# Kernel optimization log

Hardware: AMD Instinct MI355X
Metric: run time of the kernel (lower is better)

## Reference

```python
import jax, jax.numpy as jnp
import numpy as np

N = 100000   # num nodes
E = 1200000  # num edges
D = 64       # embedding dim
K = 3        # propagation hops (alpha has K+1 entries)


def setup_inputs() -> dict:
    key = jax.random.key(0)
    k1, k2, k3 = jax.random.split(key, 3)
    edge_index = jax.random.randint(k1, (2, E), 0, N, dtype=jnp.int64)
    weight = jax.random.normal(k2, (N, D), dtype=jnp.float32)
    alpha = jax.random.uniform(k3, (K + 1,), dtype=jnp.float32)
    return {"edge_index": edge_index, "weight": weight, "alpha": alpha}


def reference(edge_index, weight, alpha):
    row = edge_index[0]  # source j
    col = edge_index[1]  # target i
    # symmetric normalization: in-degree over col, deg^-1/2 with inf -> 0
    deg = jax.ops.segment_sum(jnp.ones((E,), dtype=weight.dtype), col, num_segments=N)
    dinv = jnp.where(deg == 0, 0.0, deg ** -0.5)
    edge_w = dinv[row] * dinv[col]  # [E]

    out = weight * alpha[0]
    x = weight
    for k in range(1, K + 1):
        # gather-scale-scatter propagation hop
        msg = edge_w[:, None] * x[row]                      # [E, D]
        x = jax.ops.segment_sum(msg, col, num_segments=N)   # [N, D]
        out = out + x * alpha[k]

    # per-edge link scores: dot(out[src], out[dst])
    return jnp.sum(out[row] * out[col], axis=-1)  # [E]
```

## Files before the change

kernel.cpp:

```cpp
#include <hip/hip_runtime.h>
#include <hip/hip_bf16.h>

#define GN 100000
#define GE 1200000
#define GD 64
#define NG 256
#define CPG 391
#define CAP 6144
#define PADCAP 12032
#define ZROFF (GN << 7)


__global__ void detect_kernel(const void* __restrict__ w,
                              const void* __restrict__ edge,
                              int* __restrict__ flags, int* __restrict__ gcount,
                              __hip_bfloat16* __restrict__ X,
                              __hip_bfloat16* __restrict__ Y) {
    __shared__ int s_badw, s_edgenz;
    if (threadIdx.x == 0) { s_badw = 0; s_edgenz = 0; }
    gcount[threadIdx.x] = 0;
    if (threadIdx.x < 16) {
        uint2 z; z.x = 0u; z.y = 0u;
        *(uint2*)(X + (size_t)GN * GD + 4 * threadIdx.x) = z;
        *(uint2*)(Y + (size_t)GN * GD + 4 * threadIdx.x) = z;
    }
    __syncthreads();
    const unsigned short* wh = (const unsigned short*)w;
    const unsigned int*   ei = (const unsigned int*)edge;
    int badw = 0, edgenz = 0;
    for (int i = threadIdx.x; i < 4096; i += 256) {
        unsigned int bits = ((unsigned int)wh[i]) << 16;
        float v = __uint_as_float(bits);
        if (!(fabsf(v) <= 100.0f)) badw = 1;
        if ((i & 1) == 1 && ei[i] != 0u) edgenz = 1;
    }
    if (badw)   atomicOr(&s_badw, 1);
    if (edgenz) atomicOr(&s_edgenz, 1);
    __syncthreads();
    if (threadIdx.x == 0) {
        flags[0] = s_badw ? 0 : 1;
        flags[1] = s_edgenz ? 0 : 1;
    }
}

__device__ __forceinline__ int ld_row(const int* __restrict__ edge, int e, int e64) {
    return e64 ? edge[2 * (size_t)e] : edge[e];
}
__device__ __forceinline__ int ld_col(const int* __restrict__ edge, int e, int e64) {
    return e64 ? edge[2 * ((size_t)GE + (size_t)e)] : edge[(size_t)GE + (size_t)e];
}
__device__ __forceinline__ float ld_f(const void* __restrict__ p, size_t i, int bf16f) {
    if (bf16f) return __bfloat162float(((const __hip_bfloat16*)p)[i]);
    return ((const float*)p)[i];
}

__device__ __forceinline__ float bf_lo(unsigned u) { return __uint_as_float(u << 16); }
__device__ __forceinline__ float bf_hi(unsigned u) { return __uint_as_float(u & 0xFFFF0000u); }
__device__ __forceinline__ unsigned bf16bits(float f) {
    __hip_bfloat16 h = __float2bfloat16(f);
    unsigned short s;
    __builtin_memcpy(&s, &h, 2);
    return (unsigned)s;
}

__global__ void p1init_kernel(const int* __restrict__ edge, const int* __restrict__ flags,
                              int* __restrict__ gcount, unsigned* __restrict__ bucket,
                              int E, int chunk,
                              const void* __restrict__ w, const void* __restrict__ alpha,
                              __hip_bfloat16* __restrict__ OUT, int nd) {
    if (blockIdx.x < NG) {
        __shared__ int cnt[NG];
        __shared__ int base[NG];
        int t = threadIdx.x;
        int e64 = flags[1];
        cnt[t] = 0;
        __syncthreads();
        int lo = blockIdx.x * chunk;
        int hiE = min(lo + chunk, E);
        for (int e = lo + t; e < hiE; e += 256) {
            int c = ld_col(edge, e, e64);
            int r = ld_row(edge, e, e64);
            if ((unsigned)c < (unsigned)GN && (unsigned)r < (unsigned)GN)
                atomicAdd(&cnt[c / CPG], 1);
        }
        __syncthreads();
        int cv = cnt[t];
        base[t] = (cv > 0) ? atomicAdd(&gcount[t], cv) : 0;
        __syncthreads();
        cnt[t] = 0;
        __syncthreads();
        for (int e = lo + t; e < hiE; e += 256) {
            int c = ld_col(edge, e, e64);
            int r = ld_row(edge, e, e64);
            if ((unsigned)c < (unsigned)GN && (unsigned)r < (unsigned)GN) {
                int g = c / CPG;
                int idx = base[g] + atomicAdd(&cnt[g], 1);
                if (idx < CAP)
                    bucket[(size_t)g * CAP + idx] = ((unsigned)(c - g * CPG) << 17) | (unsigned)r;
            }
        }
    } else {
        int bid = blockIdx.x - NG;
        int i = 4 * (bid * 256 + (int)threadIdx.x);
        int wbf = flags[0];
        if (i < nd) {
            float a0 = ld_f(alpha, 0, wbf);
            float v0 = ld_f(w, i + 0, wbf);
            float v1 = ld_f(w, i + 1, wbf);
            float v2 = ld_f(w, i + 2, wbf);
            float v3 = ld_f(w, i + 3, wbf);
            uint2 oq;
            oq.x = (bf16bits(a0 * v1) << 16) | bf16bits(a0 * v0);
            oq.y = (bf16bits(a0 * v3) << 16) | bf16bits(a0 * v2);
            *(uint2*)(OUT + i) = oq;
        }
    }
}

__global__ void p2_kernel(const unsigned* __restrict__ bucket, const int* __restrict__ gcount,
                          int2* __restrict__ begend, float* __restrict__ dinv,
                          int* __restrict__ csr,
                          const void* __restrict__ w, const int* __restrict__ flags,
                          __hip_bfloat16* __restrict__ XS) {
    int g = blockIdx.x;
    int t = threadIdx.x;
    __shared__ int hist[512];
    __shared__ int s[512];
    __shared__ float sdv[512];
    hist[t] = 0; hist[t + 256] = 0;
    __syncthreads();
    int mg = gcount[g]; if (mg > CAP) mg = CAP;
    const unsigned* bk = bucket + (size_t)g * CAP;
    for (int idx = t; idx < mg; idx += 256)
        atomicAdd(&hist[bk[idx] >> 17], 1);
    __syncthreads();
    int h0 = hist[t], h1 = hist[t + 256];
    int p0 = (h0 + 15) & ~15;
    int p1 = (h1 + 15) & ~15;
    s[t] = p0; s[t + 256] = p1;
    __syncthreads();
    for (int off = 1; off < 512; off <<= 1) {
        int v0 = (t >= off) ? s[t - off] : 0;
        int v1 = (t + 256 >= off) ? s[t + 256 - off] : 0;
        __syncthreads();
        s[t] += v0; s[t + 256] += v1;
        __syncthreads();
    }
    int gb = g * PADCAP;
    int beg0 = gb + s[t] - p0;
    int beg1 = gb + s[t + 256] - p1;
    float dv0 = (h0 > 0) ? rsqrtf((float)h0) : 0.0f;
    float dv1 = (h1 > 0) ? rsqrtf((float)h1) : 0.0f;
    sdv[t] = dv0; sdv[t + 256] = dv1;
    int col0 = g * CPG + t;
    int col1 = col0 + 256;
    if (col0 < GN) {
        begend[col0] = make_int2(beg0, beg0 + p0);
        dinv[col0] = dv0;
    }
    if (t + 256 < CPG && col1 < GN) {
        begend[col1] = make_int2(beg1, beg1 + p1);
        dinv[col1] = dv1;
    }
    __syncthreads();
    hist[t] = s[t] - p0;
    hist[t + 256] = s[t + 256] - p1;
    __syncthreads();
    for (int idx = t; idx < mg; idx += 256) {
        unsigned u = bk[idx];
        int cl = u >> 17;
        int r  = (int)(u & 0x1FFFFu);
        int pos = gb + atomicAdd(&hist[cl], 1);
        csr[pos] = r << 7;
    }
    if (col0 < GN)
        for (int q = h0; q < p0; ++q) csr[beg0 + q] = ZROFF;
    if (t + 256 < CPG && col1 < GN)
        for (int q = h1; q < p1; ++q) csr[beg1 + q] = ZROFF;
    int lo = g * CPG;
    int ncols = min(CPG, GN - lo);
    int tot = ncols << 6;
    int wbf = flags[0];
    size_t gbase = (size_t)lo << 6;
    if (wbf) {
        const unsigned short* wp = (const unsigned short*)w;
        for (int idx = 4 * t; idx < tot; idx += 1024) {
            float dv = sdv[idx >> 6];
            size_t base = gbase + (size_t)idx;
            uint2 wv = *(const uint2*)(wp + base);
            uint2 o;
            o.x = (bf16bits(dv * bf_hi(wv.x)) << 16) | bf16bits(dv * bf_lo(wv.x));
            o.y = (bf16bits(dv * bf_hi(wv.y)) << 16) | bf16bits(dv * bf_lo(wv.y));
            *(uint2*)(XS + base) = o;
        }
    } else {
        const float* wp = (const float*)w;
        for (int idx = 4 * t; idx < tot; idx += 1024) {
            float dv = sdv[idx >> 6];
            size_t base = gbase + (size_t)idx;
            float4 wv = *(const float4*)(wp + base);
            uint2 o;
            o.x = (bf16bits(dv * wv.y) << 16) | bf16bits(dv * wv.x);
            o.y = (bf16bits(dv * wv.w) << 16) | bf16bits(dv * wv.z);
            *(uint2*)(XS + base) = o;
        }
    }
}

__device__ __forceinline__ void acc16(int rv, unsigned ioff, const char* __restrict__ xb,
                                      int h, float& f0, float& f1, float& f2, float& f3) {
    unsigned r0 = (unsigned)__shfl(rv, h,      16);
    unsigned r1 = (unsigned)__shfl(rv, 4 + h,  16);
    unsigned r2 = (unsigned)__shfl(rv, 8 + h,  16);
    unsigned r3 = (unsigned)__shfl(rv, 12 + h, 16);
    uint2 u0 = *(const uint2*)(xb + (r0 + ioff));
    uint2 u1 = *(const uint2*)(xb + (r1 + ioff));
    uint2 u2 = *(const uint2*)(xb + (r2 + ioff));
    uint2 u3 = *(const uint2*)(xb + (r3 + ioff));
    f0 += bf_lo(u0.x); f1 += bf_hi(u0.x); f2 += bf_lo(u0.y); f3 += bf_hi(u0.y);
    f0 += bf_lo(u1.x); f1 += bf_hi(u1.x); f2 += bf_lo(u1.y); f3 += bf_hi(u1.y);
    f0 += bf_lo(u2.x); f1 += bf_hi(u2.x); f2 += bf_lo(u2.y); f3 += bf_hi(u2.y);
    f0 += bf_lo(u3.x); f1 += bf_hi(u3.x); f2 += bf_lo(u3.y); f3 += bf_hi(u3.y);
}

__global__ void gather_kernel(const __hip_bfloat16* __restrict__ XS,
                              __hip_bfloat16* __restrict__ Y,
                              __hip_bfloat16* __restrict__ OUT,
                              const int2* __restrict__ begend, const int* __restrict__ csr,
                              const float* __restrict__ dinv,
                              const void* __restrict__ alpha, const int* __restrict__ flags,
                              int k, int store_y, int N, int W) {
    int t = blockIdx.x * blockDim.x + threadIdx.x;
    int wid = __builtin_amdgcn_readfirstlane(t >> 6);
    if (wid >= N) return;
    int lane = t & 63;
    int h = lane >> 4;
    int i = lane & 15;
    float a = ld_f(alpha, k, flags[0]);
    const char* xb = (const char*)XS;
    unsigned ioff = 8u * (unsigned)i;
    int node = wid;
    int2 be = begend[node];
    float dc = dinv[node];
    size_t obase = (size_t)node * GD + 4 * i;
    uint2 uo = *(const uint2*)(OUT + obase);
    int rv = csr[be.x + i];
    for (;;) {
        int nn = node + W;
        bool more = nn < N;
        int2 be_n = make_int2(0, 0);
        float dc_n = 0.0f;
        uint2 uo_n; uo_n.x = 0u; uo_n.y = 0u;
        int rv_n = 0;
        if (more) {
            be_n = begend[nn];
            dc_n = dinv[nn];
            uo_n = *(const uint2*)(OUT + (size_t)nn * GD + 4 * i);
        }
        float f0 = 0.0f, f1 = 0.0f, f2 = 0.0f, f3 = 0.0f;
        int j = be.x;
        if (j < be.y) {
            acc16(rv, ioff, xb, h, f0, f1, f2, f3);
            for (j += 16; j < be.y; j += 16)
                acc16(csr[j + i], ioff, xb, h, f0, f1, f2, f3);
        }
        if (more) rv_n = csr[be_n.x + i];
        f0 += __shfl_xor(f0, 16, 64); f0 += __shfl_xor(f0, 32, 64);
        f1 += __shfl_xor(f1, 16, 64); f1 += __shfl_xor(f1, 32, 64);
        f2 += __shfl_xor(f2, 16, 64); f2 += __shfl_xor(f2, 32, 64);
        f3 += __shfl_xor(f3, 16, 64); f3 += __shfl_xor(f3, 32, 64);
        f0 *= dc; f1 *= dc; f2 *= dc; f3 *= dc;
        if (h == 0) {
            if (store_y) {
                uint2 p;
                p.x = (bf16bits(dc * f1) << 16) | bf16bits(dc * f0);
                p.y = (bf16bits(dc * f3) << 16) | bf16bits(dc * f2);
                *(uint2*)(Y + obase) = p;
            }
            float o0 = fmaf(a, f0, bf_lo(uo.x));
            float o1 = fmaf(a, f1, bf_hi(uo.x));
            float o2 = fmaf(a, f2, bf_lo(uo.y));
            float o3 = fmaf(a, f3, bf_hi(uo.y));
            uint2 q;
            q.x = (bf16bits(o1) << 16) | bf16bits(o0);
            q.y = (bf16bits(o3) << 16) | bf16bits(o2);
            *(uint2*)(OUT + obase) = q;
        }
        if (!more) break;
        node = nn; be = be_n; dc = dc_n; uo = uo_n; rv = rv_n;
        obase = (size_t)node * GD + 4 * i;
    }
}

__device__ __forceinline__ float dot2_bf16(unsigned ua, unsigned ub) {
    return fmaf(bf_lo(ua), bf_lo(ub), bf_hi(ua) * bf_hi(ub));
}

__global__ void dot_kernel(const __hip_bfloat16* __restrict__ OUT,
                           const int* __restrict__ edge, const int* __restrict__ flags,
                           void* __restrict__ res, int E, int NQ) {
    int t = blockIdx.x * blockDim.x + threadIdx.x;
    int q = t >> 2;
    int sub = t & 3;
    if (q >= E) return;
    int e64 = flags[1];
    int wbf = flags[0];
    int e0 = q;
    int r0 = ld_row(edge, e0, e64);
    int c0 = ld_col(edge, e0, e64);
    float m0 = ((unsigned)r0 < (unsigned)GN && (unsigned)c0 < (unsigned)GN) ? 1.0f : 0.0f;
    unsigned rc = ((unsigned)r0 < (unsigned)GN) ? (unsigned)r0 : 0u;
    unsigned cc = ((unsigned)c0 < (unsigned)GN) ? (unsigned)c0 : 0u;
    const uint4* pa = (const uint4*)(OUT + (size_t)rc * GD + sub * 16);
    const uint4* pb = (const uint4*)(OUT + (size_t)cc * GD + sub * 16);
    uint4 a0 = pa[0], a1 = pa[1], b0 = pb[0], b1 = pb[1];
    int e1 = e0 + NQ;
    bool more1 = e1 < E;
    int r1 = 0, c1 = 0;
    if (more1) { r1 = ld_row(edge, e1, e64); c1 = ld_col(edge, e1, e64); }
    for (;;) {
        uint4 na0, na1, nb0, nb1;
        na0.x=na0.y=na0.z=na0.w=0u; na1=na0; nb0=na0; nb1=na0;
        float m1 = 0.0f;
        if (more1) {
            m1 = ((unsigned)r1 < (unsigned)GN && (unsigned)c1 < (unsigned)GN) ? 1.0f : 0.0f;
            unsigned rc1 = ((unsigned)r1 < (unsigned)GN) ? (unsigned)r1 : 0u;
            unsigned cc1 = ((unsigned)c1 < (unsigned)GN) ? (unsigned)c1 : 0u;
            const uint4* qa = (const uint4*)(OUT + (size_t)rc1 * GD + sub * 16);
            const uint4* qb = (const uint4*)(OUT + (size_t)cc1 * GD + sub * 16);
            na0 = qa[0]; na1 = qa[1]; nb0 = qb[0]; nb1 = qb[1];
        }
        int e2 = e1 + NQ;
        bool more2 = more1 && (e2 < E);
        int r2 = 0, c2 = 0;
        if (more2) { r2 = ld_row(edge, e2, e64); c2 = ld_col(edge, e2, e64); }
        float p = (((dot2_bf16(a0.x, b0.x) + dot2_bf16(a0.y, b0.y)) +
                    (dot2_bf16(a0.z, b0.z) + dot2_bf16(a0.w, b0.w))) +
                   ((dot2_bf16(a1.x, b1.x) + dot2_bf16(a1.y, b1.y)) +
                    (dot2_bf16(a1.z, b1.z) + dot2_bf16(a1.w, b1.w)))) * m0;
        p += __shfl_down(p, 2, 4);
        p += __shfl_down(p, 1, 4);
        if (sub == 0) {
            if (wbf) ((__hip_bfloat16*)res)[e0] = __float2bfloat16(p);
            else     ((float*)res)[e0] = p;
        }
        if (!more1) break;
        e0 = e1; m0 = m1;
        a0 = na0; a1 = na1; b0 = nb0; b1 = nb1;
        e1 = e2; more1 = more2; r1 = r2; c1 = c2;
    }
}

extern "C" void kernel_launch(void* const* d_in, const int* in_sizes, int n_in,
                              void* d_out, int out_size, void* d_ws, size_t ws_size,
                              hipStream_t stream) {
    const int E = GE, N = GN, ND = GN * GD;
    const int NDP = (GN + 1) * GD;

    const void* edge   = d_in[0];
    const void* weight = d_in[1];
    const void* alpha  = d_in[2];

    char* ws = (char*)d_ws;
    int*      flags     = (int*)ws;      ws += 256;
    int*      gcount    = (int*)ws;      ws += 1024;
    float*    dinv      = (float*)ws;    ws += (((size_t)N * 4 + 255) / 256) * 256;
    int2*     begend    = (int2*)ws;     ws += (((size_t)N * 8 + 255) / 256) * 256;
    unsigned* bucket    = (unsigned*)ws; ws += (size_t)NG * CAP * 4;
    int*      csr       = (int*)ws;      ws += (size_t)NG * PADCAP * 4;
    __hip_bfloat16* X   = (__hip_bfloat16*)ws; ws += (size_t)NDP * 2;
    __hip_bfloat16* Y   = (__hip_bfloat16*)ws; ws += (size_t)NDP * 2;
    __hip_bfloat16* OUT = (__hip_bfloat16*)ws; ws += (size_t)ND * 2;

    const int B = 256;

    detect_kernel<<<1, 256, 0, stream>>>(weight, edge, flags, gcount, X, Y);

    {
        const int chunk = (E + NG - 1) / NG;
        const int initBlocks = (ND / 4 + B - 1) / B;
        p1init_kernel<<<NG + initBlocks, B, 0, stream>>>(
            (const int*)edge, flags, gcount, bucket, E, chunk,
            weight, alpha, OUT, ND);
    }
    p2_kernel<<<NG, 256, 0, stream>>>(bucket, gcount, begend, dinv, csr,
                                      weight, flags, X);

    const int PB = 2048;
    const int W  = PB * (B / 64);
    gather_kernel<<<PB, B, 0, stream>>>(X, Y, OUT, begend, csr, dinv, alpha, flags, 1, 1, N, W);
    gather_kernel<<<PB, B, 0, stream>>>(Y, X, OUT, begend, csr, dinv, alpha, flags, 2, 1, N, W);
    gather_kernel<<<PB, B, 0, stream>>>(X, Y, OUT, begend, csr, dinv, alpha, flags, 3, 0, N, W);

    const int NQ = PB * B / 4;
    dot_kernel<<<PB, B, 0, stream>>>(OUT, (const int*)edge, flags, d_out, E, NQ);
}
```

Before: 245.3 us.

## Widen gather to 8 lanes per row with 16-byte loads and 8-padded CSR

The gather kernel now uses 8 lanes of 16-byte loads per neighbor row instead of 16 lanes of 8-byte loads, so each wavefront processes 8 neighbors at a time. Neighbor indices are fetched 64 at a time and broadcast with full-wave shuffles, and the final reduction uses three xor steps. CSR segments are padded to multiples of 8 instead of 16, which shrinks padding and the CSR footprint, and the init kernel writes 8 bf16 per thread. The goal is fewer memory instructions and less padded-edge work, at the cost of more accumulator registers, a longer reduction, and reads of index slots past the segment end, which the extra workspace slack covers.

Measured after the change: 276.2 us. 12.6% more time.

```diff
diff --git a/kernel.cpp b/kernel.cpp
--- a/kernel.cpp
+++ b/kernel.cpp
@@ -7,7 +7,7 @@
 #define NG 256
 #define CPG 391
 #define CAP 6144
-#define PADCAP 12032
+#define PADCAP 8960
 #define ZROFF (GN << 7)
 
 
@@ -101,7 +101,7 @@
         }
     } else {
         int bid = blockIdx.x - NG;
-        int i = 4 * (bid * 256 + (int)threadIdx.x);
+        int i = 8 * (bid * 256 + (int)threadIdx.x);
         int wbf = flags[0];
         if (i < nd) {
             float a0 = ld_f(alpha, 0, wbf);
@@ -109,10 +109,16 @@
             float v1 = ld_f(w, i + 1, wbf);
             float v2 = ld_f(w, i + 2, wbf);
             float v3 = ld_f(w, i + 3, wbf);
-            uint2 oq;
+            float v4 = ld_f(w, i + 4, wbf);
+            float v5 = ld_f(w, i + 5, wbf);
+            float v6 = ld_f(w, i + 6, wbf);
+            float v7 = ld_f(w, i + 7, wbf);
+            uint4 oq;
             oq.x = (bf16bits(a0 * v1) << 16) | bf16bits(a0 * v0);
             oq.y = (bf16bits(a0 * v3) << 16) | bf16bits(a0 * v2);
-            *(uint2*)(OUT + i) = oq;
+            oq.z = (bf16bits(a0 * v5) << 16) | bf16bits(a0 * v4);
+            oq.w = (bf16bits(a0 * v7) << 16) | bf16bits(a0 * v6);
+            *(uint4*)(OUT + i) = oq;
         }
     }
 }
@@ -135,8 +141,8 @@
         atomicAdd(&hist[bk[idx] >> 17], 1);
     __syncthreads();
     int h0 = hist[t], h1 = hist[t + 256];
-    int p0 = (h0 + 15) & ~15;
-    int p1 = (h1 + 15) & ~15;
+    int p0 = (h0 + 7) & ~7;
+    int p1 = (h1 + 7) & ~7;
     s[t] = p0; s[t + 256] = p1;
     __syncthreads();
     for (int off = 1; off < 512; off <<= 1) {
@@ -207,22 +213,6 @@
     }
 }
 
-__device__ __forceinline__ void acc16(int rv, unsigned ioff, const char* __restrict__ xb,
-                                      int h, float& f0, float& f1, float& f2, float& f3) {
-    unsigned r0 = (unsigned)__shfl(rv, h,      16);
-    unsigned r1 = (unsigned)__shfl(rv, 4 + h,  16);
-    unsigned r2 = (unsigned)__shfl(rv, 8 + h,  16);
-    unsigned r3 = (unsigned)__shfl(rv, 12 + h, 16);
-    uint2 u0 = *(const uint2*)(xb + (r0 + ioff));
-    uint2 u1 = *(const uint2*)(xb + (r1 + ioff));
-    uint2 u2 = *(const uint2*)(xb + (r2 + ioff));
-    uint2 u3 = *(const uint2*)(xb + (r3 + ioff));
-    f0 += bf_lo(u0.x); f1 += bf_hi(u0.x); f2 += bf_lo(u0.y); f3 += bf_hi(u0.y);
-    f0 += bf_lo(u1.x); f1 += bf_hi(u1.x); f2 += bf_lo(u1.y); f3 += bf_hi(u1.y);
-    f0 += bf_lo(u2.x); f1 += bf_hi(u2.x); f2 += bf_lo(u2.y); f3 += bf_hi(u2.y);
-    f0 += bf_lo(u3.x); f1 += bf_hi(u3.x); f2 += bf_lo(u3.y); f3 += bf_hi(u3.y);
-}
-
 __global__ void gather_kernel(const __hip_bfloat16* __restrict__ XS,
                               __hip_bfloat16* __restrict__ Y,
                               __hip_bfloat16* __restrict__ OUT,
@@ -234,61 +224,84 @@
     int wid = __builtin_amdgcn_readfirstlane(t >> 6);
     if (wid >= N) return;
     int lane = t & 63;
-    int h = lane >> 4;
-    int i = lane & 15;
+    int h = lane >> 3;
+    int i = lane & 7;
     float a = ld_f(alpha, k, flags[0]);
     const char* xb = (const char*)XS;
-    unsigned ioff = 8u * (unsigned)i;
+    unsigned ioff = 16u * (unsigned)i;
     int node = wid;
     int2 be = begend[node];
     float dc = dinv[node];
-    size_t obase = (size_t)node * GD + 4 * i;
-    uint2 uo = *(const uint2*)(OUT + obase);
-    int rv = csr[be.x + i];
+    size_t obase = (size_t)node * GD + 8 * i;
+    uint4 uo = *(const uint4*)(OUT + obase);
+    int rv = csr[be.x + lane];
     for (;;) {
         int nn = node + W;
         bool more = nn < N;
         int2 be_n = make_int2(0, 0);
         float dc_n = 0.0f;
-        uint2 uo_n; uo_n.x = 0u; uo_n.y = 0u;
+        uint4 uo_n; uo_n.x = uo_n.y = uo_n.z = uo_n.w = 0u;
         int rv_n = 0;
         if (more) {
             be_n = begend[nn];
             dc_n = dinv[nn];
-            uo_n = *(const uint2*)(OUT + (size_t)nn * GD + 4 * i);
-        }
-        float f0 = 0.0f, f1 = 0.0f, f2 = 0.0f, f3 = 0.0f;
-        int j = be.x;
-        if (j < be.y) {
-            acc16(rv, ioff, xb, h, f0, f1, f2, f3);
-            for (j += 16; j < be.y; j += 16)
-                acc16(csr[j + i], ioff, xb, h, f0, f1, f2, f3);
-        }
-        if (more) rv_n = csr[be_n.x + i];
-        f0 += __shfl_xor(f0, 16, 64); f0 += __shfl_xor(f0, 32, 64);
-        f1 += __shfl_xor(f1, 16, 64); f1 += __shfl_xor(f1, 32, 64);
-        f2 += __shfl_xor(f2, 16, 64); f2 += __shfl_xor(f2, 32, 64);
-        f3 += __shfl_xor(f3, 16, 64); f3 += __shfl_xor(f3, 32, 64);
+            uo_n = *(const uint4*)(OUT + (size_t)nn * GD + 8 * i);
+        }
+        float f0 = 0.f, f1 = 0.f, f2 = 0.f, f3 = 0.f;
+        float f4 = 0.f, f5 = 0.f, f6 = 0.f, f7 = 0.f;
+        int base = be.x;
+        for (;;) {
+            int cnt = min(64, be.y - base);
+            for (int s = 0; s < cnt; s += 8) {
+                unsigned r = (unsigned)__shfl(rv, s + h, 64);
+                uint4 u = *(const uint4*)(xb + (r + ioff));
+                f0 += bf_lo(u.x); f1 += bf_hi(u.x);
+                f2 += bf_lo(u.y); f3 += bf_hi(u.y);
+                f4 += bf_lo(u.z); f5 += bf_hi(u.z);
+                f6 += bf_lo(u.w); f7 += bf_hi(u.w);
+            }
+            base += 64;
+            if (base >= be.y) break;
+            rv = csr[base + lane];
+        }
+        if (more) rv_n = csr[be_n.x + lane];
+        f0 += __shfl_xor(f0, 8, 64); f0 += __shfl_xor(f0, 16, 64); f0 += __shfl_xor(f0, 32, 64);
+        f1 += __shfl_xor(f1, 8, 64); f1 += __shfl_xor(f1, 16, 64); f1 += __shfl_xor(f1, 32, 64);
+        f2 += __shfl_xor(f2, 8, 64); f2 += __shfl_xor(f2, 16, 64); f2 += __shfl_xor(f2, 32, 64);
+        f3 += __shfl_xor(f3, 8, 64); f3 += __shfl_xor(f3, 16, 64); f3 += __shfl_xor(f3, 32, 64);
+        f4 += __shfl_xor(f4, 8, 64); f4 += __shfl_xor(f4, 16, 64); f4 += __shfl_xor(f4, 32, 64);
+        f5 += __shfl_xor(f5, 8, 64); f5 += __shfl_xor(f5, 16, 64); f5 += __shfl_xor(f5, 32, 64);
+        f6 += __shfl_xor(f6, 8, 64); f6 += __shfl_xor(f6, 16, 64); f6 += __shfl_xor(f6, 32, 64);
+        f7 += __shfl_xor(f7, 8, 64); f7 += __shfl_xor(f7, 16, 64); f7 += __shfl_xor(f7, 32, 64);
         f0 *= dc; f1 *= dc; f2 *= dc; f3 *= dc;
+        f4 *= dc; f5 *= dc; f6 *= dc; f7 *= dc;
         if (h == 0) {
             if (store_y) {
-                uint2 p;
+                uint4 p;
                 p.x = (bf16bits(dc * f1) << 16) | bf16bits(dc * f0);
                 p.y = (bf16bits(dc * f3) << 16) | bf16bits(dc * f2);
-                *(uint2*)(Y + obase) = p;
+                p.z = (bf16bits(dc * f5) << 16) | bf16bits(dc * f4);
+                p.w = (bf16bits(dc * f7) << 16) | bf16bits(dc * f6);
+                *(uint4*)(Y + obase) = p;
             }
             float o0 = fmaf(a, f0, bf_lo(uo.x));
             float o1 = fmaf(a, f1, bf_hi(uo.x));
             float o2 = fmaf(a, f2, bf_lo(uo.y));
             float o3 = fmaf(a, f3, bf_hi(uo.y));
-            uint2 q;
+            float o4 = fmaf(a, f4, bf_lo(uo.z));
+            float o5 = fmaf(a, f5, bf_hi(uo.z));
+            float o6 = fmaf(a, f6, bf_lo(uo.w));
+            float o7 = fmaf(a, f7, bf_hi(uo.w));
+            uint4 q;
             q.x = (bf16bits(o1) << 16) | bf16bits(o0);
             q.y = (bf16bits(o3) << 16) | bf16bits(o2);
-            *(uint2*)(OUT + obase) = q;
+            q.z = (bf16bits(o5) << 16) | bf16bits(o4);
+            q.w = (bf16bits(o7) << 16) | bf16bits(o6);
+            *(uint4*)(OUT + obase) = q;
         }
         if (!more) break;
         node = nn; be = be_n; dc = dc_n; uo = uo_n; rv = rv_n;
-        obase = (size_t)node * GD + 4 * i;
+        obase = (size_t)node * GD + 8 * i;
     }
 }
 
@@ -367,7 +380,7 @@
     float*    dinv      = (float*)ws;    ws += (((size_t)N * 4 + 255) / 256) * 256;
     int2*     begend    = (int2*)ws;     ws += (((size_t)N * 8 + 255) / 256) * 256;
     unsigned* bucket    = (unsigned*)ws; ws += (size_t)NG * CAP * 4;
-    int*      csr       = (int*)ws;      ws += (size_t)NG * PADCAP * 4;
+    int*      csr       = (int*)ws;      ws += (size_t)NG * PADCAP * 4 + 256;
     __hip_bfloat16* X   = (__hip_bfloat16*)ws; ws += (size_t)NDP * 2;
     __hip_bfloat16* Y   = (__hip_bfloat16*)ws; ws += (size_t)NDP * 2;
     __hip_bfloat16* OUT = (__hip_bfloat16*)ws; ws += (size_t)ND * 2;
@@ -378,7 +391,7 @@
 
     {
         const int chunk = (E + NG - 1) / NG;
-        const int initBlocks = (ND / 4 + B - 1) / B;
+        const int initBlocks = (ND / 8 + B - 1) / B;
         p1init_kernel<<<NG + initBlocks, B, 0, stream>>>(
             (const int*)edge, flags, gcount, bucket, E, chunk,
             weight, alpha, OUT, ND);
```

## Assign contiguous node/edge ranges per wave and prefetch first neighbor rows

Applied to the files above, without the earlier changes.

Gather waves now process a contiguous block of nodes instead of a grid stride. They also issue the first 16 neighbor-row loads for the next node before finishing the current one, overlapping that latency with the reduction and store. The dot kernel likewise walks contiguous edge ranges per quad, and the init path writes 8 bf16 values per thread with 16-byte stores. Launch bounds are added to the gather kernel, and the csr buffer is padded so the speculative prefetch cannot read past its end. The prefetch adds register pressure, and contiguous partitioning can worsen load balance or coalescing of edge-index reads.

After: 272.6 us. +11.1%, slower.

```diff
diff --git a/kernel.cpp b/kernel.cpp
--- a/kernel.cpp
+++ b/kernel.cpp
@@ -101,7 +101,7 @@
         }
     } else {
         int bid = blockIdx.x - NG;
-        int i = 4 * (bid * 256 + (int)threadIdx.x);
+        int i = 8 * (bid * 256 + (int)threadIdx.x);
         int wbf = flags[0];
         if (i < nd) {
             float a0 = ld_f(alpha, 0, wbf);
@@ -109,10 +109,16 @@
             float v1 = ld_f(w, i + 1, wbf);
             float v2 = ld_f(w, i + 2, wbf);
             float v3 = ld_f(w, i + 3, wbf);
-            uint2 oq;
+            float v4 = ld_f(w, i + 4, wbf);
+            float v5 = ld_f(w, i + 5, wbf);
+            float v6 = ld_f(w, i + 6, wbf);
+            float v7 = ld_f(w, i + 7, wbf);
+            uint4 oq;
             oq.x = (bf16bits(a0 * v1) << 16) | bf16bits(a0 * v0);
             oq.y = (bf16bits(a0 * v3) << 16) | bf16bits(a0 * v2);
-            *(uint2*)(OUT + i) = oq;
+            oq.z = (bf16bits(a0 * v5) << 16) | bf16bits(a0 * v4);
+            oq.w = (bf16bits(a0 * v7) << 16) | bf16bits(a0 * v6);
+            *(uint4*)(OUT + i) = oq;
         }
     }
 }
@@ -223,35 +229,49 @@
     f0 += bf_lo(u3.x); f1 += bf_hi(u3.x); f2 += bf_lo(u3.y); f3 += bf_hi(u3.y);
 }
 
-__global__ void gather_kernel(const __hip_bfloat16* __restrict__ XS,
-                              __hip_bfloat16* __restrict__ Y,
-                              __hip_bfloat16* __restrict__ OUT,
-                              const int2* __restrict__ begend, const int* __restrict__ csr,
-                              const float* __restrict__ dinv,
-                              const void* __restrict__ alpha, const int* __restrict__ flags,
-                              int k, int store_y, int N, int W) {
+__global__ void __launch_bounds__(256, 8)
+gather_kernel(const __hip_bfloat16* __restrict__ XS,
+              __hip_bfloat16* __restrict__ Y,
+              __hip_bfloat16* __restrict__ OUT,
+              const int2* __restrict__ begend, const int* __restrict__ csr,
+              const float* __restrict__ dinv,
+              const void* __restrict__ alpha, const int* __restrict__ flags,
+              int k, int store_y, int N, int npw) {
     int t = blockIdx.x * blockDim.x + threadIdx.x;
     int wid = __builtin_amdgcn_readfirstlane(t >> 6);
-    if (wid >= N) return;
+    int n0 = wid * npw;
+    if (n0 >= N) return;
+    int nend = min(n0 + npw, N);
     int lane = t & 63;
     int h = lane >> 4;
     int i = lane & 15;
     float a = ld_f(alpha, k, flags[0]);
     const char* xb = (const char*)XS;
     unsigned ioff = 8u * (unsigned)i;
-    int node = wid;
+    int node = n0;
     int2 be = begend[node];
     float dc = dinv[node];
     size_t obase = (size_t)node * GD + 4 * i;
     uint2 uo = *(const uint2*)(OUT + obase);
     int rv = csr[be.x + i];
+    uint2 p0, p1, p2, p3;
+    p0.x = p0.y = p1.x = p1.y = p2.x = p2.y = p3.x = p3.y = 0u;
+    if (be.x < be.y) {
+        unsigned r0 = (unsigned)__shfl(rv, h,      16);
+        unsigned r1 = (unsigned)__shfl(rv, 4 + h,  16);
+        unsigned r2 = (unsigned)__shfl(rv, 8 + h,  16);
+        unsigned r3 = (unsigned)__shfl(rv, 12 + h, 16);
+        p0 = *(const uint2*)(xb + (r0 + ioff));
+        p1 = *(const uint2*)(xb + (r1 + ioff));
+        p2 = *(const uint2*)(xb + (r2 + ioff));
+        p3 = *(const uint2*)(xb + (r3 + ioff));
+    }
     for (;;) {
-        int nn = node + W;
-        bool more = nn < N;
+        int nn = node + 1;
+        bool more = nn < nend;
         int2 be_n = make_int2(0, 0);
         float dc_n = 0.0f;
         uint2 uo_n; uo_n.x = 0u; uo_n.y = 0u;
-        int rv_n = 0;
         if (more) {
             be_n = begend[nn];
             dc_n = dinv[nn];
@@ -260,16 +280,32 @@
         float f0 = 0.0f, f1 = 0.0f, f2 = 0.0f, f3 = 0.0f;
         int j = be.x;
         if (j < be.y) {
-            acc16(rv, ioff, xb, h, f0, f1, f2, f3);
+            f0 += bf_lo(p0.x); f1 += bf_hi(p0.x); f2 += bf_lo(p0.y); f3 += bf_hi(p0.y);
+            f0 += bf_lo(p1.x); f1 += bf_hi(p1.x); f2 += bf_lo(p1.y); f3 += bf_hi(p1.y);
+            f0 += bf_lo(p2.x); f1 += bf_hi(p2.x); f2 += bf_lo(p2.y); f3 += bf_hi(p2.y);
+            f0 += bf_lo(p3.x); f1 += bf_hi(p3.x); f2 += bf_lo(p3.y); f3 += bf_hi(p3.y);
             for (j += 16; j < be.y; j += 16)
                 acc16(csr[j + i], ioff, xb, h, f0, f1, f2, f3);
         }
+        int rv_n = 0;
         if (more) rv_n = csr[be_n.x + i];
         f0 += __shfl_xor(f0, 16, 64); f0 += __shfl_xor(f0, 32, 64);
         f1 += __shfl_xor(f1, 16, 64); f1 += __shfl_xor(f1, 32, 64);
         f2 += __shfl_xor(f2, 16, 64); f2 += __shfl_xor(f2, 32, 64);
         f3 += __shfl_xor(f3, 16, 64); f3 += __shfl_xor(f3, 32, 64);
         f0 *= dc; f1 *= dc; f2 *= dc; f3 *= dc;
+        uint2 q0, q1, q2, q3;
+        q0.x = q0.y = q1.x = q1.y = q2.x = q2.y = q3.x = q3.y = 0u;
+        if (more && be_n.x < be_n.y) {
+            unsigned r0 = (unsigned)__shfl(rv_n, h,      16);
+            unsigned r1 = (unsigned)__shfl(rv_n, 4 + h,  16);
+            unsigned r2 = (unsigned)__shfl(rv_n, 8 + h,  16);
+            unsigned r3 = (unsigned)__shfl(rv_n, 12 + h, 16);
+            q0 = *(const uint2*)(xb + (r0 + ioff));
+            q1 = *(const uint2*)(xb + (r1 + ioff));
+            q2 = *(const uint2*)(xb + (r2 + ioff));
+            q3 = *(const uint2*)(xb + (r3 + ioff));
+        }
         if (h == 0) {
             if (store_y) {
                 uint2 p;
@@ -287,7 +323,8 @@
             *(uint2*)(OUT + obase) = q;
         }
         if (!more) break;
-        node = nn; be = be_n; dc = dc_n; uo = uo_n; rv = rv_n;
+        node = nn; be = be_n; dc = dc_n; uo = uo_n;
+        p0 = q0; p1 = q1; p2 = q2; p3 = q3;
         obase = (size_t)node * GD + 4 * i;
     }
 }
@@ -298,14 +335,15 @@
 
 __global__ void dot_kernel(const __hip_bfloat16* __restrict__ OUT,
                            const int* __restrict__ edge, const int* __restrict__ flags,
-                           void* __restrict__ res, int E, int NQ) {
+                           void* __restrict__ res, int E, int epq) {
     int t = blockIdx.x * blockDim.x + threadIdx.x;
     int q = t >> 2;
     int sub = t & 3;
-    if (q >= E) return;
+    int e0 = q * epq;
+    if (e0 >= E) return;
+    int eend = min(e0 + epq, E);
     int e64 = flags[1];
     int wbf = flags[0];
-    int e0 = q;
     int r0 = ld_row(edge, e0, e64);
     int c0 = ld_col(edge, e0, e64);
     float m0 = ((unsigned)r0 < (unsigned)GN && (unsigned)c0 < (unsigned)GN) ? 1.0f : 0.0f;
@@ -314,8 +352,8 @@
     const uint4* pa = (const uint4*)(OUT + (size_t)rc * GD + sub * 16);
     const uint4* pb = (const uint4*)(OUT + (size_t)cc * GD + sub * 16);
     uint4 a0 = pa[0], a1 = pa[1], b0 = pb[0], b1 = pb[1];
-    int e1 = e0 + NQ;
-    bool more1 = e1 < E;
+    int e1 = e0 + 1;
+    bool more1 = e1 < eend;
     int r1 = 0, c1 = 0;
     if (more1) { r1 = ld_row(edge, e1, e64); c1 = ld_col(edge, e1, e64); }
     for (;;) {
@@ -330,8 +368,8 @@
             const uint4* qb = (const uint4*)(OUT + (size_t)cc1 * GD + sub * 16);
             na0 = qa[0]; na1 = qa[1]; nb0 = qb[0]; nb1 = qb[1];
         }
-        int e2 = e1 + NQ;
-        bool more2 = more1 && (e2 < E);
+        int e2 = e1 + 1;
+        bool more2 = more1 && (e2 < eend);
         int r2 = 0, c2 = 0;
         if (more2) { r2 = ld_row(edge, e2, e64); c2 = ld_col(edge, e2, e64); }
         float p = (((dot2_bf16(a0.x, b0.x) + dot2_bf16(a0.y, b0.y)) +
@@ -367,7 +405,7 @@
     float*    dinv      = (float*)ws;    ws += (((size_t)N * 4 + 255) / 256) * 256;
     int2*     begend    = (int2*)ws;     ws += (((size_t)N * 8 + 255) / 256) * 256;
     unsigned* bucket    = (unsigned*)ws; ws += (size_t)NG * CAP * 4;
-    int*      csr       = (int*)ws;      ws += (size_t)NG * PADCAP * 4;
+    int*      csr       = (int*)ws;      ws += (size_t)NG * PADCAP * 4 + 256;
     __hip_bfloat16* X   = (__hip_bfloat16*)ws; ws += (size_t)NDP * 2;
     __hip_bfloat16* Y   = (__hip_bfloat16*)ws; ws += (size_t)NDP * 2;
     __hip_bfloat16* OUT = (__hip_bfloat16*)ws; ws += (size_t)ND * 2;
@@ -378,7 +416,7 @@
 
     {
         const int chunk = (E + NG - 1) / NG;
-        const int initBlocks = (ND / 4 + B - 1) / B;
+        const int initBlocks = (ND / 8 + B - 1) / B;
         p1init_kernel<<<NG + initBlocks, B, 0, stream>>>(
             (const int*)edge, flags, gcount, bucket, E, chunk,
             weight, alpha, OUT, ND);
@@ -388,10 +426,12 @@
 
     const int PB = 2048;
     const int W  = PB * (B / 64);
-    gather_kernel<<<PB, B, 0, stream>>>(X, Y, OUT, begend, csr, dinv, alpha, flags, 1, 1, N, W);
-    gather_kernel<<<PB, B, 0, stream>>>(Y, X, OUT, begend, csr, dinv, alpha, flags, 2, 1, N, W);
-    gather_kernel<<<PB, B, 0, stream>>>(X, Y, OUT, begend, csr, dinv, alpha, flags, 3, 0, N, W);
+    const int npw = (N + W - 1) / W;
+    gather_kernel<<<PB, B, 0, stream>>>(X, Y, OUT, begend, csr, dinv, alpha, flags, 1, 1, N, npw);
+    gather_kernel<<<PB, B, 0, stream>>>(Y, X, OUT, begend, csr, dinv, alpha, flags, 2, 1, N, npw);
+    gather_kernel<<<PB, B, 0, stream>>>(X, Y, OUT, begend, csr, dinv, alpha, flags, 3, 0, N, npw);
 
     const int NQ = PB * B / 4;
-    dot_kernel<<<PB, B, 0, stream>>>(OUT, (const int*)edge, flags, d_out, E, NQ);
-}
+    const int epq = (E + NQ - 1) / NQ;
+    dot_kernel<<<PB, B, 0, stream>>>(OUT, (const int*)edge, flags, d_out, E, epq);
+}
```

## Fuse three propagation hops and dot into one cooperative persistent kernel

Applied to the files above, without the earlier changes.

Replaces the three gather launches and the dot launch with a single cooperative kernel that uses grid.sync between phases. Each wave keeps its partial OUT accumulator in registers across hops instead of re-reading and re-writing OUT in global memory, and writes OUT only in the final hop. The init path is also widened to 8 elements per thread with 16-byte stores. The costs are grid-wide barrier latency, register pressure from the per-node out[NPW] array (NPW=13 or 25), and a runtime occupancy check that falls back to the old path.

Result: slower. 252.0 us (+2.7%).

```diff
diff --git a/kernel.cpp b/kernel.cpp
--- a/kernel.cpp
+++ b/kernel.cpp
@@ -1,5 +1,6 @@
 #include <hip/hip_runtime.h>
 #include <hip/hip_bf16.h>
+#include <hip/hip_cooperative_groups.h>
 
 #define GN 100000
 #define GE 1200000
@@ -10,6 +11,8 @@
 #define PADCAP 12032
 #define ZROFF (GN << 7)
 
+
+namespace cg = cooperative_groups;
 
 __global__ void detect_kernel(const void* __restrict__ w,
                               const void* __restrict__ edge,
@@ -101,7 +104,7 @@
         }
     } else {
         int bid = blockIdx.x - NG;
-        int i = 4 * (bid * 256 + (int)threadIdx.x);
+        int i = 8 * (bid * 256 + (int)threadIdx.x);
         int wbf = flags[0];
         if (i < nd) {
             float a0 = ld_f(alpha, 0, wbf);
@@ -109,10 +112,16 @@
             float v1 = ld_f(w, i + 1, wbf);
             float v2 = ld_f(w, i + 2, wbf);
             float v3 = ld_f(w, i + 3, wbf);
-            uint2 oq;
+            float v4 = ld_f(w, i + 4, wbf);
+            float v5 = ld_f(w, i + 5, wbf);
+            float v6 = ld_f(w, i + 6, wbf);
+            float v7 = ld_f(w, i + 7, wbf);
+            uint4 oq;
             oq.x = (bf16bits(a0 * v1) << 16) | bf16bits(a0 * v0);
             oq.y = (bf16bits(a0 * v3) << 16) | bf16bits(a0 * v2);
-            *(uint2*)(OUT + i) = oq;
+            oq.z = (bf16bits(a0 * v5) << 16) | bf16bits(a0 * v4);
+            oq.w = (bf16bits(a0 * v7) << 16) | bf16bits(a0 * v6);
+            *(uint4*)(OUT + i) = oq;
         }
     }
 }
@@ -221,6 +230,160 @@
     f0 += bf_lo(u1.x); f1 += bf_hi(u1.x); f2 += bf_lo(u1.y); f3 += bf_hi(u1.y);
     f0 += bf_lo(u2.x); f1 += bf_hi(u2.x); f2 += bf_lo(u2.y); f3 += bf_hi(u2.y);
     f0 += bf_lo(u3.x); f1 += bf_hi(u3.x); f2 += bf_lo(u3.y); f3 += bf_hi(u3.y);
+}
+
+template<int NPW, bool FIRST, bool STORE, bool WOUT>
+__device__ __forceinline__ void hop_phase(const char* __restrict__ xb,
+        __hip_bfloat16* __restrict__ DST,
+        __hip_bfloat16* __restrict__ OUT,
+        const int2* __restrict__ begend, const int* __restrict__ csr,
+        const float* __restrict__ dinv, float a,
+        int wid, int W, int N, int h, int i, unsigned ioff,
+        uint2 (&out)[NPW])
+{
+    int node = wid;
+    int2 be = begend[node];
+    float dc = dinv[node];
+    size_t obase = (size_t)node * GD + 4 * i;
+    uint2 uo = FIRST ? *(const uint2*)(OUT + obase) : out[0];
+    int rv = csr[be.x + i];
+    #pragma unroll
+    for (int tt = 0; tt < NPW; ++tt) {
+        int nn = node + W;
+        bool more = (tt + 1 < NPW) && (nn < N);
+        int2 be_n = make_int2(0, 0);
+        float dc_n = 0.0f;
+        uint2 uo_n; uo_n.x = 0u; uo_n.y = 0u;
+        if (more) {
+            be_n = begend[nn];
+            dc_n = dinv[nn];
+            if (FIRST) uo_n = *(const uint2*)(OUT + (size_t)nn * GD + 4 * i);
+            else       uo_n = out[(tt + 1 < NPW) ? tt + 1 : 0];
+        }
+        float f0 = 0.0f, f1 = 0.0f, f2 = 0.0f, f3 = 0.0f;
+        int j = be.x;
+        if (j < be.y) {
+            acc16(rv, ioff, xb, h, f0, f1, f2, f3);
+            for (j += 16; j < be.y; j += 16)
+                acc16(csr[j + i], ioff, xb, h, f0, f1, f2, f3);
+        }
+        int rv_n = 0;
+        if (more) rv_n = csr[be_n.x + i];
+        f0 += __shfl_xor(f0, 16, 64); f0 += __shfl_xor(f0, 32, 64);
+        f1 += __shfl_xor(f1, 16, 64); f1 += __shfl_xor(f1, 32, 64);
+        f2 += __shfl_xor(f2, 16, 64); f2 += __shfl_xor(f2, 32, 64);
+        f3 += __shfl_xor(f3, 16, 64); f3 += __shfl_xor(f3, 32, 64);
+        f0 *= dc; f1 *= dc; f2 *= dc; f3 *= dc;
+        if (STORE && h == 0) {
+            uint2 p;
+            p.x = (bf16bits(dc * f1) << 16) | bf16bits(dc * f0);
+            p.y = (bf16bits(dc * f3) << 16) | bf16bits(dc * f2);
+            *(uint2*)(DST + obase) = p;
+        }
+        float o0 = fmaf(a, f0, bf_lo(uo.x));
+        float o1 = fmaf(a, f1, bf_hi(uo.x));
+        float o2 = fmaf(a, f2, bf_lo(uo.y));
+        float o3 = fmaf(a, f3, bf_hi(uo.y));
+        uint2 acc;
+        acc.x = (bf16bits(o1) << 16) | bf16bits(o0);
+        acc.y = (bf16bits(o3) << 16) | bf16bits(o2);
+        if (WOUT) {
+            if (h == 0) *(uint2*)(OUT + obase) = acc;
+        } else {
+            out[tt] = acc;
+        }
+        if (!more) break;
+        node = nn; be = be_n; dc = dc_n; uo = uo_n; rv = rv_n;
+        obase = (size_t)node * GD + 4 * i;
+    }
+}
+
+__device__ __forceinline__ float dot2_bf16(unsigned ua, unsigned ub) {
+    return fmaf(bf_lo(ua), bf_lo(ub), bf_hi(ua) * bf_hi(ub));
+}
+
+__device__ __forceinline__ void dot_body(const __hip_bfloat16* __restrict__ OUT,
+        const int* __restrict__ edge, int e64, int wbf,
+        void* __restrict__ res, int E, int NQ, int t) {
+    int q = t >> 2;
+    int sub = t & 3;
+    if (q >= E) return;
+    int e0 = q;
+    int r0 = ld_row(edge, e0, e64);
+    int c0 = ld_col(edge, e0, e64);
+    float m0 = ((unsigned)r0 < (unsigned)GN && (unsigned)c0 < (unsigned)GN) ? 1.0f : 0.0f;
+    unsigned rc = ((unsigned)r0 < (unsigned)GN) ? (unsigned)r0 : 0u;
+    unsigned cc = ((unsigned)c0 < (unsigned)GN) ? (unsigned)c0 : 0u;
+    const uint4* pa = (const uint4*)(OUT + (size_t)rc * GD + sub * 16);
+    const uint4* pb = (const uint4*)(OUT + (size_t)cc * GD + sub * 16);
+    uint4 a0 = pa[0], a1 = pa[1], b0 = pb[0], b1 = pb[1];
+    int e1 = e0 + NQ;
+    bool more1 = e1 < E;
+    int r1 = 0, c1 = 0;
+    if (more1) { r1 = ld_row(edge, e1, e64); c1 = ld_col(edge, e1, e64); }
+    for (;;) {
+        uint4 na0, na1, nb0, nb1;
+        na0.x=na0.y=na0.z=na0.w=0u; na1=na0; nb0=na0; nb1=na0;
+        float m1 = 0.0f;
+        if (more1) {
+            m1 = ((unsigned)r1 < (unsigned)GN && (unsigned)c1 < (unsigned)GN) ? 1.0f : 0.0f;
+            unsigned rc1 = ((unsigned)r1 < (unsigned)GN) ? (unsigned)r1 : 0u;
+            unsigned cc1 = ((unsigned)c1 < (unsigned)GN) ? (unsigned)c1 : 0u;
+            const uint4* qa = (const uint4*)(OUT + (size_t)rc1 * GD + sub * 16);
+            const uint4* qb = (const uint4*)(OUT + (size_t)cc1 * GD + sub * 16);
+            na0 = qa[0]; na1 = qa[1]; nb0 = qb[0]; nb1 = qb[1];
+        }
+        int e2 = e1 + NQ;
+        bool more2 = more1 && (e2 < E);
+        int r2 = 0, c2 = 0;
+        if (more2) { r2 = ld_row(edge, e2, e64); c2 = ld_col(edge, e2, e64); }
+        float p = (((dot2_bf16(a0.x, b0.x) + dot2_bf16(a0.y, b0.y)) +
+                    (dot2_bf16(a0.z, b0.z) + dot2_bf16(a0.w, b0.w))) +
+                   ((dot2_bf16(a1.x, b1.x) + dot2_bf16(a1.y, b1.y)) +
+                    (dot2_bf16(a1.z, b1.z) + dot2_bf16(a1.w, b1.w)))) * m0;
+        p += __shfl_down(p, 2, 4);
+        p += __shfl_down(p, 1, 4);
+        if (sub == 0) {
+            if (wbf) ((__hip_bfloat16*)res)[e0] = __float2bfloat16(p);
+            else     ((float*)res)[e0] = p;
+        }
+        if (!more1) break;
+        e0 = e1; m0 = m1;
+        a0 = na0; a1 = na1; b0 = nb0; b1 = nb1;
+        e1 = e2; more1 = more2; r1 = r2; c1 = c2;
+    }
+}
+
+template<int NPW, int WPE>
+__global__ void __launch_bounds__(256, WPE)
+fused_kernel(__hip_bfloat16* X, __hip_bfloat16* Y, __hip_bfloat16* OUT,
+             const int2* begend, const int* csr, const float* dinv,
+             const void* alpha, const int* flags,
+             const int* edge, void* res, int N, int E, int W)
+{
+    cg::grid_group grid = cg::this_grid();
+    int t = blockIdx.x * blockDim.x + threadIdx.x;
+    int wid = __builtin_amdgcn_readfirstlane(t >> 6);
+    int lane = t & 63;
+    int h = lane >> 4;
+    int i = lane & 15;
+    unsigned ioff = 8u * (unsigned)i;
+    int wbf = flags[0];
+    int e64 = flags[1];
+    float a1 = ld_f(alpha, 1, wbf);
+    float a2 = ld_f(alpha, 2, wbf);
+    float a3 = ld_f(alpha, 3, wbf);
+    uint2 out[NPW];
+    hop_phase<NPW, true,  true,  false>((const char*)X, Y, OUT, begend, csr, dinv, a1, wid, W, N, h, i, ioff, out);
+    __threadfence();
+    grid.sync();
+    hop_phase<NPW, false, true,  false>((const char*)Y, X, OUT, begend, csr, dinv, a2, wid, W, N, h, i, ioff, out);
+    __threadfence();
+    grid.sync();
+    hop_phase<NPW, false, false, true >((const char*)X, Y, OUT, begend, csr, dinv, a3, wid, W, N, h, i, ioff, out);
+    __threadfence();
+    grid.sync();
+    dot_body(OUT, edge, e64, wbf, res, E, (int)(gridDim.x * blockDim.x) / 4, t);
 }
 
 __global__ void gather_kernel(const __hip_bfloat16* __restrict__ XS,
@@ -292,63 +455,11 @@
     }
 }
 
-__device__ __forceinline__ float dot2_bf16(unsigned ua, unsigned ub) {
-    return fmaf(bf_lo(ua), bf_lo(ub), bf_hi(ua) * bf_hi(ub));
-}
-
 __global__ void dot_kernel(const __hip_bfloat16* __restrict__ OUT,
                            const int* __restrict__ edge, const int* __restrict__ flags,
                            void* __restrict__ res, int E, int NQ) {
     int t = blockIdx.x * blockDim.x + threadIdx.x;
-    int q = t >> 2;
-    int sub = t & 3;
-    if (q >= E) return;
-    int e64 = flags[1];
-    int wbf = flags[0];
-    int e0 = q;
-    int r0 = ld_row(edge, e0, e64);
-    int c0 = ld_col(edge, e0, e64);
-    float m0 = ((unsigned)r0 < (unsigned)GN && (unsigned)c0 < (unsigned)GN) ? 1.0f : 0.0f;
-    unsigned rc = ((unsigned)r0 < (unsigned)GN) ? (unsigned)r0 : 0u;
-    unsigned cc = ((unsigned)c0 < (unsigned)GN) ? (unsigned)c0 : 0u;
-    const uint4* pa = (const uint4*)(OUT + (size_t)rc * GD + sub * 16);
-    const uint4* pb = (const uint4*)(OUT + (size_t)cc * GD + sub * 16);
-    uint4 a0 = pa[0], a1 = pa[1], b0 = pb[0], b1 = pb[1];
-    int e1 = e0 + NQ;
-    bool more1 = e1 < E;
-    int r1 = 0, c1 = 0;
-    if (more1) { r1 = ld_row(edge, e1, e64); c1 = ld_col(edge, e1, e64); }
-    for (;;) {
-        uint4 na0, na1, nb0, nb1;
-        na0.x=na0.y=na0.z=na0.w=0u; na1=na0; nb0=na0; nb1=na0;
-        float m1 = 0.0f;
-        if (more1) {
-            m1 = ((unsigned)r1 < (unsigned)GN && (unsigned)c1 < (unsigned)GN) ? 1.0f : 0.0f;
-            unsigned rc1 = ((unsigned)r1 < (unsigned)GN) ? (unsigned)r1 : 0u;
-            unsigned cc1 = ((unsigned)c1 < (unsigned)GN) ? (unsigned)c1 : 0u;
-            const uint4* qa = (const uint4*)(OUT + (size_t)rc1 * GD + sub * 16);
-            const uint4* qb = (const uint4*)(OUT + (size_t)cc1 * GD + sub * 16);
-            na0 = qa[0]; na1 = qa[1]; nb0 = qb[0]; nb1 = qb[1];
-        }
-        int e2 = e1 + NQ;
-        bool more2 = more1 && (e2 < E);
-        int r2 = 0, c2 = 0;
-        if (more2) { r2 = ld_row(edge, e2, e64); c2 = ld_col(edge, e2, e64); }
-        float p = (((dot2_bf16(a0.x, b0.x) + dot2_bf16(a0.y, b0.y)) +
-                    (dot2_bf16(a0.z, b0.z) + dot2_bf16(a0.w, b0.w))) +
-                   ((dot2_bf16(a1.x, b1.x) + dot2_bf16(a1.y, b1.y)) +
-                    (dot2_bf16(a1.z, b1.z) + dot2_bf16(a1.w, b1.w)))) * m0;
-        p += __shfl_down(p, 2, 4);
-        p += __shfl_down(p, 1, 4);
-        if (sub == 0) {
-            if (wbf) ((__hip_bfloat16*)res)[e0] = __float2bfloat16(p);
-            else     ((float*)res)[e0] = p;
-        }
-        if (!more1) break;
-        e0 = e1; m0 = m1;
-        a0 = na0; a1 = na1; b0 = nb0; b1 = nb1;
-        e1 = e2; more1 = more2; r1 = r2; c1 = c2;
-    }
+    dot_body(OUT, edge, flags[1], flags[0], res, E, NQ, t);
 }
 
 extern "C" void kernel_launch(void* const* d_in, const int* in_sizes, int n_in,
@@ -367,7 +478,7 @@
     float*    dinv      = (float*)ws;    ws += (((size_t)N * 4 + 255) / 256) * 256;
     int2*     begend    = (int2*)ws;     ws += (((size_t)N * 8 + 255) / 256) * 256;
     unsigned* bucket    = (unsigned*)ws; ws += (size_t)NG * CAP * 4;
-    int*      csr       = (int*)ws;      ws += (size_t)NG * PADCAP * 4;
+    int*      csr       = (int*)ws;      ws += (size_t)NG * PADCAP * 4 + 256;
     __hip_bfloat16* X   = (__hip_bfloat16*)ws; ws += (size_t)NDP * 2;
     __hip_bfloat16* Y   = (__hip_bfloat16*)ws; ws += (size_t)NDP * 2;
     __hip_bfloat16* OUT = (__hip_bfloat16*)ws; ws += (size_t)ND * 2;
@@ -378,7 +489,7 @@
 
     {
         const int chunk = (E + NG - 1) / NG;
-        const int initBlocks = (ND / 4 + B - 1) / B;
+        const int initBlocks = (ND / 8 + B - 1) / B;
         p1init_kernel<<<NG + initBlocks, B, 0, stream>>>(
             (const int*)edge, flags, gcount, bucket, E, chunk,
             weight, alpha, OUT, ND);
@@ -386,12 +497,41 @@
     p2_kernel<<<NG, 256, 0, stream>>>(bucket, gcount, begend, dinv, csr,
                                       weight, flags, X);
 
-    const int PB = 2048;
-    const int W  = PB * (B / 64);
-    gather_kernel<<<PB, B, 0, stream>>>(X, Y, OUT, begend, csr, dinv, alpha, flags, 1, 1, N, W);
-    gather_kernel<<<PB, B, 0, stream>>>(Y, X, OUT, begend, csr, dinv, alpha, flags, 2, 1, N, W);
-    gather_kernel<<<PB, B, 0, stream>>>(X, Y, OUT, begend, csr, dinv, alpha, flags, 3, 0, N, W);
-
-    const int NQ = PB * B / 4;
-    dot_kernel<<<PB, B, 0, stream>>>(OUT, (const int*)edge, flags, d_out, E, NQ);
-}
+    static int path = -1;
+    if (path < 0) {
+        int nb = 0;
+        if (hipOccupancyMaxActiveBlocksPerMultiprocessor(&nb, fused_kernel<13, 8>, 256, 0) == hipSuccess && nb >= 8)
+            path = 0;
+        else {
+            nb = 0;
+            if (hipOccupancyMaxActiveBlocksPerMultiprocessor(&nb, fused_kernel<25, 4>, 256, 0) == hipSuccess && nb >= 4)
+                path = 1;
+            else
+                path = 2;
+        }
+    }
+
+    if (path == 0 || path == 1) {
+        int PB = (path == 0) ? 2048 : 1024;
+        int W  = PB * (B / 64);
+        int Nn = N, Ee = E;
+        __hip_bfloat16* Xp = X; __hip_bfloat16* Yp = Y; __hip_bfloat16* Op = OUT;
+        const int2* bep = begend; const int* csrp = csr; const float* dvp = dinv;
+        const void* alp = alpha; const int* flp = flags;
+        const int* edp = (const int*)edge; void* resp = d_out;
+        void* kargs[] = {&Xp, &Yp, &Op, &bep, &csrp, &dvp, &alp, &flp,
+                         &edp, &resp, &Nn, &Ee, &W};
+        if (path == 0)
+            hipLaunchCooperativeKernel(fused_kernel<13, 8>, dim3(PB), dim3(B), kargs, 0, stream);
+        else
+            hipLaunchCooperativeKernel(fused_kernel<25, 4>, dim3(PB), dim3(B), kargs, 0, stream);
+    } else {
+        const int PB = 2048;
+        const int W  = PB * (B / 64);
+        gather_kernel<<<PB, B, 0, stream>>>(X, Y, OUT, begend, csr, dinv, alpha, flags, 1, 1, N, W);
+        gather_kernel<<<PB, B, 0, stream>>>(Y, X, OUT, begend, csr, dinv, alpha, flags, 2, 1, N, W);
+        gather_kernel<<<PB, B, 0, stream>>>(X, Y, OUT, begend, csr, dinv, alpha, flags, 3, 0, N, W);
+        const int NQ = PB * B / 4;
+        dot_kernel<<<PB, B, 0, stream>>>(OUT, (const int*)edge, flags, d_out, E, NQ);
+    }
+}
```
